# Kernel tuning notes

Measured on AMD Instinct MI355X. Metric: run time of the kernel, lower is better.

The kernel has to match this reference:

```python
import jax, jax.numpy as jnp
import numpy as np

DIM = 2048
RANK = 128


def _xavier_uniform(key, shape, gain=0.5):
    fan_out, fan_in = shape
    limit = gain * np.sqrt(6.0 / (fan_in + fan_out))
    return jax.random.uniform(key, shape, jnp.float32, -limit, limit)


def setup_inputs() -> dict:
    key = jax.random.key(0)
    ks = jax.random.split(key, 6)
    T, B = 1024, 16
    x = jax.random.normal(ks[0], (T, B, DIM), jnp.float32)
    h0 = jax.random.normal(ks[1], (B, DIM), jnp.float32)
    U_x = _xavier_uniform(ks[2], (DIM, RANK))
    V_x = _xavier_uniform(ks[3], (RANK, DIM))
    U_d = _xavier_uniform(ks[4], (DIM, RANK))
    V_d = _xavier_uniform(ks[5], (RANK, DIM))
    r_h = jnp.full((DIM,), 0.9, jnp.float32)
    r_delta = jnp.full((DIM,), 0.1, jnp.float32)
    b = jnp.zeros((DIM,), jnp.float32)
    b_delta = jnp.full((DIM,), -2.0, jnp.float32)
    b_gate = jnp.zeros((DIM,), jnp.float32)
    return {"x": x, "h0": h0, "U_x": U_x, "V_x": V_x, "U_d": U_d, "V_d": V_d,
            "r_h": r_h, "r_delta": r_delta, "b": b, "b_delta": b_delta, "b_gate": b_gate}


def reference(x, h0, U_x, V_x, U_d, V_d, r_h, r_delta, b, b_delta, b_gate):
    # Precompute input projections for all timesteps (batched low-rank GEMMs):
    # W(x) = U @ (V @ x)  ->  [T,B,D]
    wx = jnp.einsum('tbd,rd,or->tbo', x, V_x, U_x)
    wd = jnp.einsum('tbd,rd,or->tbo', x, V_d, U_d)

    def step(h_prev, inp):
        x_t, wx_t, wd_t = inp
        cand = jnp.tanh(r_h * h_prev + wx_t + b)
        delta = jax.nn.sigmoid(wd_t + r_delta * h_prev + b_delta)
        h_new = (1.0 - delta) * h_prev + delta * cand
        g = h_new + x_t + b_gate
        out = h_new * (g * jax.nn.sigmoid(g))  # silu gate
        return h_new, (out, h_new)

    _, (output, hs) = jax.lax.scan(step, h0, (x, wx, wd))
    h = jnp.concatenate([h0[None], hs], axis=0)  # [T+1,B,D]
    return output, h
```

## Files before the change

### kernel.cpp

```cpp
#include <hip/hip_runtime.h>

#define DIMN 2048
#define RANKN 128
#define TT 1024
#define BBATCH 16
#define BD (BBATCH * DIMN)
#define CH 16
#define PADW 68

typedef __attribute__((ext_vector_type(4))) float floatx4;
typedef __attribute__((ext_vector_type(8))) short short8;

__device__ __forceinline__ short f2bf(float f) {
    unsigned u = __float_as_uint(f);
    unsigned r = (u + 0x7FFFu + ((u >> 16) & 1u)) >> 16;
    return (short)r;
}
__device__ __forceinline__ float fast_sigmoid(float z) {
    return 1.0f / (1.0f + __expf(-z));
}
__device__ __forceinline__ float fast_tanh(float z) {
    return 1.0f - 2.0f / (__expf(2.0f * z) + 1.0f);
}

__global__ __launch_bounds__(256)
void prep_vb(const float* __restrict__ Vx, const float* __restrict__ Vd,
             short* __restrict__ Vb) {
    const int gid = blockIdx.x * 256 + threadIdx.x;
    const size_t base = (size_t)gid * 8;
    const size_t half = (size_t)RANKN * DIMN;
    const float* src = (base < half) ? Vx : Vd;
    const size_t off = (base < half) ? base : (base - half);
    float4 a = *(const float4*)(src + off);
    float4 c = *(const float4*)(src + off + 4);
    short8 v;
    v[0] = f2bf(a.x); v[1] = f2bf(a.y); v[2] = f2bf(a.z); v[3] = f2bf(a.w);
    v[4] = f2bf(c.x); v[5] = f2bf(c.y); v[6] = f2bf(c.z); v[7] = f2bf(c.w);
    *(short8*)(Vb + base) = v;
}

__global__ __launch_bounds__(256, 2)
void gemm_xv(const float* __restrict__ X, const short* __restrict__ Vb,
             short* __restrict__ xvb) {
    constexpr int PADK = 40;
    __shared__ short As[32 * PADK];
    __shared__ short Bs[2][128 * PADK];

    const int m0 = blockIdx.x * 32;
    const int tid = threadIdx.x;
    const int wave = tid >> 6;
    const int lane = tid & 63;
    const int lr = lane & 15;
    const int q  = lane >> 4;
    const int mat = wave >> 1;
    const int wn  = (wave & 1) * 64;

    floatx4 acc[2][4] = {};

    for (int k0 = 0; k0 < DIMN; k0 += 32) {
        {
            int r = tid >> 3, c = (tid & 7) * 4;
            float4 v = *(const float4*)(X + (size_t)(m0 + r) * DIMN + k0 + c);
            *(short4*)&As[r * PADK + c] =
                make_short4(f2bf(v.x), f2bf(v.y), f2bf(v.z), f2bf(v.w));
        }
        #pragma unroll
        for (int i = 0; i < 4; ++i) {
            int u = tid + i * 256;
            int bm = u >> 9;
            int rem = u & 511;
            int r = rem >> 2, c8 = (rem & 3) * 8;
            short8 v = *(const short8*)(Vb + ((size_t)bm * RANKN + r) * DIMN + k0 + c8);
            *(short8*)&Bs[bm][r * PADK + c8] = v;
        }
        __syncthreads();

        short8 af[2], bfr[4];
        #pragma unroll
        for (int mi = 0; mi < 2; ++mi)
            af[mi] = *(const short8*)&As[(mi * 16 + lr) * PADK + q * 8];
        #pragma unroll
        for (int nj = 0; nj < 4; ++nj)
            bfr[nj] = *(const short8*)&Bs[mat][(wn + nj * 16 + lr) * PADK + q * 8];

        #pragma unroll
        for (int mi = 0; mi < 2; ++mi)
            #pragma unroll
            for (int nj = 0; nj < 4; ++nj)
                acc[mi][nj] = __builtin_amdgcn_mfma_f32_16x16x32_bf16(
                    af[mi], bfr[nj], acc[mi][nj], 0, 0, 0);
        __syncthreads();
    }

    #pragma unroll
    for (int mi = 0; mi < 2; ++mi)
        #pragma unroll
        for (int nj = 0; nj < 4; ++nj)
            #pragma unroll
            for (int r = 0; r < 4; ++r) {
                int row = m0 + mi * 16 + q * 4 + r;
                int col = mat * RANKN + wn + nj * 16 + lr;
                xvb[(size_t)row * 256 + col] = f2bf(acc[mi][nj][r]);
            }
}

__global__ __launch_bounds__(64, 1)
void fused_scan(const short* __restrict__ xvb, const float* __restrict__ x,
                const float* __restrict__ h0,
                const float* __restrict__ Ux, const float* __restrict__ Ud,
                const float* __restrict__ r_h, const float* __restrict__ r_delta,
                const float* __restrict__ bvec, const float* __restrict__ b_delta,
                const float* __restrict__ b_gate,
                float* __restrict__ obuf, float* __restrict__ hbuf) {
    __shared__ float wxs[CH * PADW];
    __shared__ float wds[CH * PADW];

    const int id   = blockIdx.x;
    const int xcd  = id & 7;
    const int slot = id >> 3;
    const int b  = xcd * 2 + (slot & 1);
    const int d0 = (slot >> 1) * 64;

    const int lane = threadIdx.x;
    const int lr = lane & 15;
    const int q  = lane >> 4;

    const int d = d0 + lane;
    const size_t xo = (size_t)b * DIMN + d;

    short8 uf[2][4][4];
    #pragma unroll
    for (int mat = 0; mat < 2; ++mat) {
        const float* Up = mat ? Ud : Ux;
        #pragma unroll
        for (int nj = 0; nj < 4; ++nj) {
            const size_t dd = (size_t)(d0 + nj * 16 + lr);
            #pragma unroll
            for (int ks = 0; ks < 4; ++ks) {
                const int k = ks * 32 + q * 8;
                float4 u0 = *(const float4*)&Up[dd * RANKN + k];
                float4 u1 = *(const float4*)&Up[dd * RANKN + k + 4];
                short8 v;
                v[0] = f2bf(u0.x); v[1] = f2bf(u0.y);
                v[2] = f2bf(u0.z); v[3] = f2bf(u0.w);
                v[4] = f2bf(u1.x); v[5] = f2bf(u1.y);
                v[6] = f2bf(u1.z); v[7] = f2bf(u1.w);
                uf[mat][nj][ks] = v;
            }
        }
    }

    const float rh  = r_h[d];
    const float rd  = r_delta[d];
    const float bb  = bvec[d];
    const float bdl = b_delta[d];
    const float bg  = b_gate[d];
    float h = h0[xo];
    hbuf[xo] = h;

    short8 afA[2][4], afB[2][4];
    float  xqA[CH],  xqB[CH];
    {
        const size_t row = (size_t)lr * BBATCH + b;
        #pragma unroll
        for (int mat = 0; mat < 2; ++mat)
            #pragma unroll
            for (int ks = 0; ks < 4; ++ks)
                afA[mat][ks] = *(const short8*)
                    &xvb[row * 256 + mat * RANKN + ks * 32 + q * 8];
        #pragma unroll
        for (int s = 0; s < CH; ++s)
            xqA[s] = x[(size_t)s * BD + xo];
    }

    auto body = [&](int ch, short8 (&afU)[2][4], short8 (&afP)[2][4],
                    float (&xU)[CH], float (&xP)[CH]) {
        if (ch < 63) {
            const size_t row = (size_t)((ch + 1) * CH + lr) * BBATCH + b;
            #pragma unroll
            for (int mat = 0; mat < 2; ++mat)
                #pragma unroll
                for (int ks = 0; ks < 4; ++ks)
                    afP[mat][ks] = *(const short8*)
                        &xvb[row * 256 + mat * RANKN + ks * 32 + q * 8];
            const size_t xb0 = (size_t)(ch + 1) * CH * BD + xo;
            #pragma unroll
            for (int s = 0; s < CH; ++s)
                xP[s] = x[xb0 + (size_t)s * BD];
        }

        #pragma unroll
        for (int mat = 0; mat < 2; ++mat) {
            float* outp = mat ? wds : wxs;
            #pragma unroll
            for (int nj = 0; nj < 4; ++nj) {
                floatx4 acc = {};
                #pragma unroll
                for (int ks = 0; ks < 4; ++ks)
                    acc = __builtin_amdgcn_mfma_f32_16x16x32_bf16(
                        afU[mat][ks], uf[mat][nj][ks], acc, 0, 0, 0);
                #pragma unroll
                for (int r = 0; r < 4; ++r)
                    outp[(q * 4 + r) * PADW + nj * 16 + lr] = acc[r];
            }
        }
        asm volatile("s_waitcnt lgkmcnt(0)" ::: "memory");

        float wxr[CH], wdr[CH];
        #pragma unroll
        for (int s = 0; s < CH; ++s) {
            wxr[s] = wxs[s * PADW + lane];
            wdr[s] = wds[s * PADW + lane];
        }

        const size_t tb = (size_t)ch * CH * BD + xo;
        #pragma unroll
        for (int s = 0; s < CH; ++s) {
            const float cand  = fast_tanh(rh * h + wxr[s] + bb);
            const float delta = fast_sigmoid(wdr[s] + rd * h + bdl);
            h = (1.0f - delta) * h + delta * cand;
            const float gg = h + xU[s] + bg;
            obuf[tb + (size_t)s * BD] = h * (gg * fast_sigmoid(gg));
            hbuf[tb + (size_t)(s + 1) * BD] = h;
        }
    };

    #pragma unroll 1
    for (int ii = 0; ii < 32; ++ii) {
        body(2 * ii,     afA, afB, xqA, xqB);
        body(2 * ii + 1, afB, afA, xqB, xqA);
    }
}

extern "C" void kernel_launch(void* const* d_in, const int* in_sizes, int n_in,
                              void* d_out, int out_size, void* d_ws, size_t ws_size,
                              hipStream_t stream) {
    const float* x       = (const float*)d_in[0];
    const float* h0      = (const float*)d_in[1];
    const float* U_x     = (const float*)d_in[2];
    const float* V_x     = (const float*)d_in[3];
    const float* U_d     = (const float*)d_in[4];
    const float* V_d     = (const float*)d_in[5];
    const float* r_h     = (const float*)d_in[6];
    const float* r_delta = (const float*)d_in[7];
    const float* bvec    = (const float*)d_in[8];
    const float* b_delta = (const float*)d_in[9];
    const float* b_gate  = (const float*)d_in[10];

    float* obuf = (float*)d_out;
    float* hbuf = obuf + (size_t)TT * BD;
    short* xvb  = (short*)d_ws;
    short* Vb   = xvb + (size_t)TT * BBATCH * 256;

    prep_vb<<<256, 256, 0, stream>>>(V_x, V_d, Vb);

    gemm_xv<<<TT * BBATCH / 32, 256, 0, stream>>>(x, Vb, xvb);

    fused_scan<<<512, 64, 0, stream>>>(xvb, x, h0, U_x, U_d,
                                       r_h, r_delta, bvec, b_delta, b_gate,
                                       obuf, hbuf);
}
```

Measured before the change: 576.5 us.

## Warp-specialize scan into MFMA producer, recurrence, and output-writer waves

Splits the single-wave scan block into three waves: one computes the low-rank U projections with MFMA into double-buffered LDS, one runs the serial recurrence, and one applies the SiLU gate and writes out/h with float4 stores. The waves hand off chunks through LDS counters with spin-waits, so the MFMA work and global stores overlap the latency-bound recurrence instead of sitting on its critical path. U fragments move from registers to LDS and the block grows to 192 threads with two blocks per CU. The cost is spin-wait overhead, extra LDS traffic, and reliance on volatile LDS flags for ordering between waves.

New measurement: 534.8 us. 1.08x faster.

```diff
diff --git a/kernel.cpp b/kernel.cpp
--- a/kernel.cpp
+++ b/kernel.cpp
@@ -104,7 +104,19 @@
             }
 }
 
-__global__ __launch_bounds__(64, 1)
+#define SPIN(ctr, tgt) \
+    while (((volatile int*)cnt)[ctr] < (tgt)) __builtin_amdgcn_s_sleep(1); \
+    asm volatile("" ::: "memory");
+
+#define SIGNAL(ctr, val) \
+    asm volatile("" ::: "memory"); \
+    if (lane == 0) ((volatile int*)cnt)[ctr] = (val);
+
+#define SIGNAL_AFTER_READS(ctr, val) \
+    asm volatile("s_waitcnt lgkmcnt(0)" ::: "memory"); \
+    if (lane == 0) ((volatile int*)cnt)[ctr] = (val);
+
+__global__ __launch_bounds__(192, 2)
 void fused_scan(const short* __restrict__ xvb, const float* __restrict__ x,
                 const float* __restrict__ h0,
                 const float* __restrict__ Ux, const float* __restrict__ Ud,
@@ -112,8 +124,11 @@
                 const float* __restrict__ bvec, const float* __restrict__ b_delta,
                 const float* __restrict__ b_gate,
                 float* __restrict__ obuf, float* __restrict__ hbuf) {
-    __shared__ float wxs[CH * PADW];
-    __shared__ float wds[CH * PADW];
+    __shared__ float wxs[2][CH * PADW];
+    __shared__ float wds[2][CH * PADW];
+    __shared__ float hsh[2][CH * PADW];
+    __shared__ short8 Ulds[2][4][4][64];
+    __shared__ int cnt[4];
 
     const int id   = blockIdx.x;
     const int xcd  = id & 7;
@@ -121,114 +136,155 @@
     const int b  = xcd * 2 + (slot & 1);
     const int d0 = (slot >> 1) * 64;
 
-    const int lane = threadIdx.x;
+    const int tid  = threadIdx.x;
+    const int wave = tid >> 6;
+    const int lane = tid & 63;
     const int lr = lane & 15;
     const int q  = lane >> 4;
 
-    const int d = d0 + lane;
-    const size_t xo = (size_t)b * DIMN + d;
-
-    short8 uf[2][4][4];
-    #pragma unroll
-    for (int mat = 0; mat < 2; ++mat) {
-        const float* Up = mat ? Ud : Ux;
-        #pragma unroll
-        for (int nj = 0; nj < 4; ++nj) {
-            const size_t dd = (size_t)(d0 + nj * 16 + lr);
-            #pragma unroll
-            for (int ks = 0; ks < 4; ++ks) {
-                const int k = ks * 32 + q * 8;
-                float4 u0 = *(const float4*)&Up[dd * RANKN + k];
-                float4 u1 = *(const float4*)&Up[dd * RANKN + k + 4];
-                short8 v;
-                v[0] = f2bf(u0.x); v[1] = f2bf(u0.y);
-                v[2] = f2bf(u0.z); v[3] = f2bf(u0.w);
-                v[4] = f2bf(u1.x); v[5] = f2bf(u1.y);
-                v[6] = f2bf(u1.z); v[7] = f2bf(u1.w);
-                uf[mat][nj][ks] = v;
-            }
-        }
-    }
-
-    const float rh  = r_h[d];
-    const float rd  = r_delta[d];
-    const float bb  = bvec[d];
-    const float bdl = b_delta[d];
-    const float bg  = b_gate[d];
-    float h = h0[xo];
-    hbuf[xo] = h;
-
-    short8 afA[2][4], afB[2][4];
-    float  xqA[CH],  xqB[CH];
-    {
-        const size_t row = (size_t)lr * BBATCH + b;
-        #pragma unroll
-        for (int mat = 0; mat < 2; ++mat)
-            #pragma unroll
-            for (int ks = 0; ks < 4; ++ks)
-                afA[mat][ks] = *(const short8*)
-                    &xvb[row * 256 + mat * RANKN + ks * 32 + q * 8];
-        #pragma unroll
-        for (int s = 0; s < CH; ++s)
-            xqA[s] = x[(size_t)s * BD + xo];
-    }
-
-    auto body = [&](int ch, short8 (&afU)[2][4], short8 (&afP)[2][4],
-                    float (&xU)[CH], float (&xP)[CH]) {
-        if (ch < 63) {
-            const size_t row = (size_t)((ch + 1) * CH + lr) * BBATCH + b;
+    if (tid == 0) { cnt[0] = 0; cnt[1] = 0; cnt[2] = 0; cnt[3] = 0; }
+    __syncthreads();
+
+    if (wave == 1) {
+        #pragma unroll
+        for (int mat = 0; mat < 2; ++mat) {
+            const float* Up = mat ? Ud : Ux;
+            #pragma unroll
+            for (int nj = 0; nj < 4; ++nj) {
+                const size_t dd = (size_t)(d0 + nj * 16 + lr);
+                #pragma unroll
+                for (int ks = 0; ks < 4; ++ks) {
+                    const int k = ks * 32 + q * 8;
+                    float4 u0 = *(const float4*)&Up[dd * RANKN + k];
+                    float4 u1 = *(const float4*)&Up[dd * RANKN + k + 4];
+                    short8 v;
+                    v[0] = f2bf(u0.x); v[1] = f2bf(u0.y);
+                    v[2] = f2bf(u0.z); v[3] = f2bf(u0.w);
+                    v[4] = f2bf(u1.x); v[5] = f2bf(u1.y);
+                    v[6] = f2bf(u1.z); v[7] = f2bf(u1.w);
+                    Ulds[mat][nj][ks][lane] = v;
+                }
+            }
+        }
+        short8 afp[2][4];
+        {
+            const size_t row = (size_t)lr * BBATCH + b;
             #pragma unroll
             for (int mat = 0; mat < 2; ++mat)
                 #pragma unroll
                 for (int ks = 0; ks < 4; ++ks)
-                    afP[mat][ks] = *(const short8*)
+                    afp[mat][ks] = *(const short8*)
                         &xvb[row * 256 + mat * RANKN + ks * 32 + q * 8];
-            const size_t xb0 = (size_t)(ch + 1) * CH * BD + xo;
-            #pragma unroll
-            for (int s = 0; s < CH; ++s)
-                xP[s] = x[xb0 + (size_t)s * BD];
-        }
-
-        #pragma unroll
-        for (int mat = 0; mat < 2; ++mat) {
-            float* outp = mat ? wds : wxs;
-            #pragma unroll
-            for (int nj = 0; nj < 4; ++nj) {
-                floatx4 acc = {};
-                #pragma unroll
-                for (int ks = 0; ks < 4; ++ks)
-                    acc = __builtin_amdgcn_mfma_f32_16x16x32_bf16(
-                        afU[mat][ks], uf[mat][nj][ks], acc, 0, 0, 0);
-                #pragma unroll
-                for (int r = 0; r < 4; ++r)
-                    outp[(q * 4 + r) * PADW + nj * 16 + lr] = acc[r];
-            }
-        }
-        asm volatile("s_waitcnt lgkmcnt(0)" ::: "memory");
-
-        float wxr[CH], wdr[CH];
-        #pragma unroll
-        for (int s = 0; s < CH; ++s) {
-            wxr[s] = wxs[s * PADW + lane];
-            wdr[s] = wds[s * PADW + lane];
-        }
-
-        const size_t tb = (size_t)ch * CH * BD + xo;
-        #pragma unroll
-        for (int s = 0; s < CH; ++s) {
-            const float cand  = fast_tanh(rh * h + wxr[s] + bb);
-            const float delta = fast_sigmoid(wdr[s] + rd * h + bdl);
-            h = (1.0f - delta) * h + delta * cand;
-            const float gg = h + xU[s] + bg;
-            obuf[tb + (size_t)s * BD] = h * (gg * fast_sigmoid(gg));
-            hbuf[tb + (size_t)(s + 1) * BD] = h;
-        }
-    };
-
-    #pragma unroll 1
-    for (int ii = 0; ii < 32; ++ii) {
-        body(2 * ii,     afA, afB, xqA, xqB);
-        body(2 * ii + 1, afB, afA, xqB, xqA);
+        }
+        for (int ch = 0; ch < 64; ++ch) {
+            if (ch >= 2) { SPIN(1, ch - 1) }
+            const int pb = ch & 1;
+            #pragma unroll
+            for (int mat = 0; mat < 2; ++mat) {
+                float* outp = mat ? wds[pb] : wxs[pb];
+                #pragma unroll
+                for (int nj = 0; nj < 4; ++nj) {
+                    floatx4 acc = {};
+                    #pragma unroll
+                    for (int ks = 0; ks < 4; ++ks)
+                        acc = __builtin_amdgcn_mfma_f32_16x16x32_bf16(
+                            afp[mat][ks], Ulds[mat][nj][ks][lane], acc, 0, 0, 0);
+                    #pragma unroll
+                    for (int r = 0; r < 4; ++r)
+                        outp[(q * 4 + r) * PADW + nj * 16 + lr] = acc[r];
+                }
+            }
+            SIGNAL(0, ch + 1)
+            if (ch < 63) {
+                const size_t row = (size_t)((ch + 1) * CH + lr) * BBATCH + b;
+                #pragma unroll
+                for (int mat = 0; mat < 2; ++mat)
+                    #pragma unroll
+                    for (int ks = 0; ks < 4; ++ks)
+                        afp[mat][ks] = *(const short8*)
+                            &xvb[row * 256 + mat * RANKN + ks * 32 + q * 8];
+            }
+        }
+    } else if (wave == 0) {
+        const int d = d0 + lane;
+        const size_t xo = (size_t)b * DIMN + d;
+        const float rh  = r_h[d];
+        const float rd  = r_delta[d];
+        const float bb  = bvec[d];
+        const float bdl = b_delta[d];
+        float h = h0[xo];
+
+        for (int ch = 0; ch < 64; ++ch) {
+            SPIN(0, ch + 1)
+            const int pb = ch & 1;
+            float wxr[CH], wdr[CH];
+            #pragma unroll
+            for (int s = 0; s < CH; ++s) {
+                wxr[s] = wxs[pb][s * PADW + lane];
+                wdr[s] = wds[pb][s * PADW + lane];
+            }
+            SIGNAL_AFTER_READS(1, ch + 1)
+            if (ch >= 2) { SPIN(3, ch - 1) }
+            #pragma unroll
+            for (int s = 0; s < CH; ++s) {
+                const float cand  = fast_tanh(rh * h + wxr[s] + bb);
+                const float delta = fast_sigmoid(wdr[s] + rd * h + bdl);
+                h = (1.0f - delta) * h + delta * cand;
+                hsh[pb][s * PADW + lane] = h;
+            }
+            SIGNAL(2, ch + 1)
+        }
+    } else {
+        const int dq  = lane & 15;
+        const int tof = lane >> 4;
+        const size_t xoffF = (size_t)b * DIMN + d0 + dq * 4;
+        const float4 bg4 = *(const float4*)&b_gate[d0 + dq * 4];
+        {
+            const int dl = d0 + lane;
+            (void)dl;
+            float4 hv = *(const float4*)&h0[(size_t)b * DIMN + d0 + dq * 4
+                                            + (size_t)tof * 0];
+            if (tof == 0)
+                *(float4*)&hbuf[(size_t)b * DIMN + d0 + dq * 4] = hv;
+        }
+        float4 xpre[4];
+        #pragma unroll
+        for (int jj = 0; jj < 4; ++jj)
+            xpre[jj] = *(const float4*)&x[(size_t)(jj * 4 + tof) * BD + xoffF];
+
+        for (int ch = 0; ch < 64; ++ch) {
+            SPIN(2, ch + 1)
+            const int pb = ch & 1;
+            float4 hv[4];
+            #pragma unroll
+            for (int jj = 0; jj < 4; ++jj)
+                hv[jj] = *(const float4*)&hsh[pb][(jj * 4 + tof) * PADW + dq * 4];
+            SIGNAL_AFTER_READS(3, ch + 1)
+            const int tb = ch * CH;
+            #pragma unroll
+            for (int jj = 0; jj < 4; ++jj) {
+                const int t = jj * 4 + tof;
+                const float4 xv = xpre[jj];
+                float4 ov;
+                float g0 = hv[jj].x + xv.x + bg4.x;
+                ov.x = hv[jj].x * (g0 * fast_sigmoid(g0));
+                float g1 = hv[jj].y + xv.y + bg4.y;
+                ov.y = hv[jj].y * (g1 * fast_sigmoid(g1));
+                float g2 = hv[jj].z + xv.z + bg4.z;
+                ov.z = hv[jj].z * (g2 * fast_sigmoid(g2));
+                float g3 = hv[jj].w + xv.w + bg4.w;
+                ov.w = hv[jj].w * (g3 * fast_sigmoid(g3));
+                *(float4*)&obuf[(size_t)(tb + t) * BD + xoffF] = ov;
+                *(float4*)&hbuf[(size_t)(tb + t + 1) * BD + xoffF] = hv[jj];
+            }
+            if (ch < 63) {
+                const int tn = (ch + 1) * CH;
+                #pragma unroll
+                for (int jj = 0; jj < 4; ++jj)
+                    xpre[jj] = *(const float4*)
+                        &x[(size_t)(tn + jj * 4 + tof) * BD + xoffF];
+            }
+        }
     }
 }
 
@@ -256,7 +312,7 @@
 
     gemm_xv<<<TT * BBATCH / 32, 256, 0, stream>>>(x, Vb, xvb);
 
-    fused_scan<<<512, 64, 0, stream>>>(xvb, x, h0, U_x, U_d,
-                                       r_h, r_delta, bvec, b_delta, b_gate,
-                                       obuf, hbuf);
-}
+    fused_scan<<<512, 192, 0, stream>>>(xvb, x, h0, U_x, U_d,
+                                        r_h, r_delta, bvec, b_delta, b_gate,
+                                        obuf, hbuf);
+}
```
